# Performance work log

Measured on AMD Instinct MI355X. Metric: run time of the kernel, lower is better.

Reference implementation:

```python
import jax, jax.numpy as jnp
import numpy as np

B, D = 16384, 1024
N_CROSS = 3
EPS = 1e-3  # keras BatchNormalization default epsilon


def _bn(x, gamma, beta, mean, var):
    # inference-mode batch norm over feature axis
    return gamma * (x - mean) * jax.lax.rsqrt(var + EPS) + beta


def setup_inputs() -> dict:
    key = jax.random.key(0)
    ks = jax.random.split(key, 16)
    s = lambda fan_in: 1.0 / np.sqrt(fan_in)
    inp = {
        "x": jax.random.normal(ks[0], (B, D), jnp.float32),
        "cross_w": jax.random.normal(ks[1], (N_CROSS, D), jnp.float32) * s(D),
        "cross_b": jax.random.normal(ks[2], (N_CROSS, D), jnp.float32) * 0.01,
        "w1": jax.random.normal(ks[3], (D, 64), jnp.float32) * s(D),
        "b1": jnp.zeros((64,), jnp.float32),
        "gamma1": jnp.ones((64,), jnp.float32),
        "beta1": jnp.zeros((64,), jnp.float32),
        "mean1": jax.random.normal(ks[4], (64,), jnp.float32) * 0.1,
        "var1": jax.random.uniform(ks[5], (64,), jnp.float32, 0.5, 1.5),
        "w2": jax.random.normal(ks[6], (64, 48), jnp.float32) * s(64),
        "b2": jnp.zeros((48,), jnp.float32),
        "gamma2": jnp.ones((48,), jnp.float32),
        "beta2": jnp.zeros((48,), jnp.float32),
        "mean2": jax.random.normal(ks[7], (48,), jnp.float32) * 0.1,
        "var2": jax.random.uniform(ks[8], (48,), jnp.float32, 0.5, 1.5),
        "w3": jax.random.normal(ks[9], (48, 24), jnp.float32) * s(48),
        "b3": jnp.zeros((24,), jnp.float32),
        "gamma3": jnp.ones((24,), jnp.float32),
        "beta3": jnp.zeros((24,), jnp.float32),
        "mean3": jax.random.normal(ks[10], (24,), jnp.float32) * 0.1,
        "var3": jax.random.uniform(ks[11], (24,), jnp.float32, 0.5, 1.5),
        "w_out": jax.random.normal(ks[12], (D + 24, 1), jnp.float32) * s(D + 24),
        "b_out": jnp.zeros((1,), jnp.float32),
    }
    return inp


def reference(x, cross_w, cross_b, w1, b1, gamma1, beta1, mean1, var1,
              w2, b2, gamma2, beta2, mean2, var2,
              w3, b3, gamma3, beta3, mean3, var3, w_out, b_out):
    # ---- cross network: xl = x0 * (xl . w) + b + xl ----
    # Algebraically identical to matmul(x0[:,:,None], xl[:,None,:]) @ w,
    # computed in O(B*D) instead of materializing [B, D, D].
    x0 = x
    xl = x
    for i in range(N_CROSS):
        scal = jnp.einsum('bd,d->b', xl, cross_w[i])  # [B]
        xl = x0 * scal[:, None] + cross_b[i] + xl
    # ---- deep tower (inference: dropout is identity, BN uses moving stats) ----
    h = _bn(jax.nn.relu(x @ w1 + b1), gamma1, beta1, mean1, var1)
    h = _bn(jnp.tanh(h @ w2 + b2), gamma2, beta2, mean2, var2)
    h = _bn(jnp.tanh(h @ w3 + b3), gamma3, beta3, mean3, var3)
    out = jnp.concatenate([xl, h], axis=1)           # [B, D+24]
    return jax.nn.sigmoid(out @ w_out + b_out)       # [B, 1]
```

## Files before the change

kernel.cpp:

```cpp
#include <hip/hip_runtime.h>
#include <hip/hip_bf16.h>
#include <math.h>

typedef __attribute__((ext_vector_type(8))) short bf16x8;
typedef __attribute__((ext_vector_type(4))) float f32x4;

constexpr int BD = 1024;
constexpr float EPS = 1e-3f;
constexpr int WB_MAIN = 32 * 5 * 64 * 8 * 2;
constexpr int WB2_OFF = WB_MAIN;
constexpr int WB3_OFF = WB2_OFF + 6144;
constexpr int CST_OFF = WB3_OFF + 4096;

__device__ __forceinline__ float wave_allsum(float v) {
#pragma unroll
    for (int m = 1; m < 64; m <<= 1) v += __shfl_xor(v, m, 64);
    return v;
}
__device__ __forceinline__ unsigned short f2bf(float f) {
    __hip_bfloat16 h = __float2bfloat16(f);
    unsigned short u; __builtin_memcpy(&u, &h, 2);
    return u;
}
__device__ __forceinline__ float bf2f(unsigned short u) {
    return __uint_as_float(((unsigned)u) << 16);
}
__device__ __forceinline__ float tanh_fast(float x) {
    const float xc = fminf(fmaxf(x, -15.f), 15.f);
    const float e = __expf(2.f * xc);
    return (e - 1.f) * __builtin_amdgcn_rcpf(e + 1.f);
}
__device__ __forceinline__ float sigmoid_fast(float z) {
    return __builtin_amdgcn_rcpf(1.f + __expf(-z));
}

__global__ void dcn_prep(const float* __restrict__ w1,
                         const float* __restrict__ cross_w,
                         const float* __restrict__ cross_b,
                         const float* __restrict__ w_out,
                         const float* __restrict__ w2,
                         const float* __restrict__ w3,
                         unsigned short* __restrict__ ws) {
    const int bx = blockIdx.x;
    if (bx == 40) {
        if (threadIdx.x < 64) {
            const int l = threadIdx.x;
            float q2 = 0.f, q3 = 0.f, Cc = 0.f;
            for (int j = 0; j < 16; ++j) {
                const int k = l * 16 + j;
                const float c0 = cross_b[k], c1 = cross_b[BD + k], c2 = cross_b[2 * BD + k];
                q2 += c0 * cross_w[BD + k];
                q3 += (c0 + c1) * cross_w[2 * BD + k];
                Cc += (c0 + c1 + c2) * w_out[k];
            }
            q2 = wave_allsum(q2); q3 = wave_allsum(q3); Cc = wave_allsum(Cc);
            float* consts = (float*)((char*)ws + CST_OFF);
            if (l == 0) { consts[0] = q2; consts[1] = q3; consts[2] = Cc; }
        }
        return;
    }
    if (bx < 40) {
        const int idx = bx * 256 + threadIdx.x;
        const int g = idx / 320;
        const int rem = idx - g * 320;
        const int t = rem >> 6;
        const int l = rem & 63;
        const int c = l & 15;
        const int k0 = g * 32 + (l >> 4) * 8;
        unsigned short o[8] __attribute__((aligned(16)));
#pragma unroll
        for (int j = 0; j < 8; ++j) {
            const int k = k0 + j;
            unsigned short r;
            if (t < 4) {
                r = f2bf(w1[k * 64 + t * 16 + c]);
            } else if (c < 8) {
                const int vsel = c & 3;
                const float v = (vsel < 3) ? cross_w[vsel * BD + k] : w_out[k];
                const unsigned short h = f2bf(v);
                r = (c < 4) ? h : f2bf(v - bf2f(h));
            } else {
                r = 0;
            }
            o[j] = r;
        }
        *(uint4*)(ws + (size_t)idx * 8) = *(const uint4*)o;
        return;
    }
    const int slot = (bx - 41) * 256 + threadIdx.x;
    if (slot < 384) {
        const int f = slot >> 6, l = slot & 63;
        const int K = f / 3, T = f % 3;
        const int kb = K * 32 + (l >> 4) * 8;
        const int col = T * 16 + (l & 15);
        unsigned short o[8] __attribute__((aligned(16)));
#pragma unroll
        for (int j = 0; j < 8; ++j) o[j] = f2bf(w2[(kb + j) * 48 + col]);
        unsigned short* wb2 = (unsigned short*)((char*)ws + WB2_OFF);
        *(uint4*)(wb2 + (size_t)slot * 8) = *(const uint4*)o;
    } else if (slot < 640) {
        const int s2 = slot - 384;
        const int f = s2 >> 6, l = s2 & 63;
        const int K = f >> 1, T = f & 1;
        const int kb = K * 32 + (l >> 4) * 8;
        const int col = T * 16 + (l & 15);
        unsigned short o[8] __attribute__((aligned(16)));
#pragma unroll
        for (int j = 0; j < 8; ++j) {
            const int k = kb + j;
            o[j] = (k < 48 && col < 24) ? f2bf(w3[k * 24 + col]) : (unsigned short)0;
        }
        unsigned short* wb3 = (unsigned short*)((char*)ws + WB3_OFF);
        *(uint4*)(wb3 + (size_t)s2 * 8) = *(const uint4*)o;
    }
}

__global__ __launch_bounds__(128, 2) void dcn_main(
    const float* __restrict__ x,
    const unsigned short* __restrict__ wbm,
    const unsigned short* __restrict__ w2f,
    const unsigned short* __restrict__ w3f,
    const float* __restrict__ consts,
    const float* __restrict__ b1, const float* __restrict__ g1,
    const float* __restrict__ be1, const float* __restrict__ m1, const float* __restrict__ v1,
    const float* __restrict__ b2, const float* __restrict__ g2,
    const float* __restrict__ be2, const float* __restrict__ m2, const float* __restrict__ v2,
    const float* __restrict__ b3, const float* __restrict__ g3,
    const float* __restrict__ be3, const float* __restrict__ m3, const float* __restrict__ v3,
    const float* __restrict__ w_out, const float* __restrict__ b_out,
    float* __restrict__ out)
{
    __shared__ char sb[14336] __attribute__((aligned(16)));
    constexpr int RED = 0, H1 = 5120, H2 = 9472, LC = 13824;

    const int tid = threadIdx.x;
    const int l = tid & 63;
    const int w = tid >> 6;
    const int ar = l & 15;
    const int ag = l >> 4;
    const int gr0 = blockIdx.x * 16;

    const float* xbase = x + (size_t)(gr0 + ar) * BD + w * 512 + ag * 8;
    const bf16x8* bb = (const bf16x8*)wbm + (size_t)(w * 16 * 5) * 64 + l;

    float4 A0[8], A1[8];
#pragma unroll
    for (int s = 0; s < 8; ++s) {
        A0[s] = *(const float4*)(xbase + s * 32);
        A1[s] = *(const float4*)(xbase + s * 32 + 4);
    }
    bf16x8 Bf[4][5];
#pragma unroll
    for (int s = 0; s < 4; ++s)
#pragma unroll
        for (int t = 0; t < 5; ++t) Bf[s][t] = bb[(s * 5 + t) * 64];

    f32x4 acc0 = {0.f,0.f,0.f,0.f}, acc1 = acc0, acc2 = acc0, acc3 = acc0, acc4 = acc0;

#pragma unroll
    for (int s = 0; s < 16; ++s) {
        const float4 va0 = A0[s & 7];
        const float4 va1 = A1[s & 7];
        if (s < 8) {
            A0[s & 7] = *(const float4*)(xbase + (s + 8) * 32);
            A1[s & 7] = *(const float4*)(xbase + (s + 8) * 32 + 4);
        }
        const bf16x8 B0 = Bf[s & 3][0], B1 = Bf[s & 3][1], B2 = Bf[s & 3][2],
                     B3 = Bf[s & 3][3], B4 = Bf[s & 3][4];
        if (s + 4 < 16) {
#pragma unroll
            for (int t = 0; t < 5; ++t) Bf[s & 3][t] = bb[((s + 4) * 5 + t) * 64];
        }
        bf16x8 xh, xl;
#define CVT(F, I) { const unsigned short h_ = f2bf(F); xh[I] = (short)h_; \
                    xl[I] = (short)f2bf((F) - bf2f(h_)); }
        CVT(va0.x, 0) CVT(va0.y, 1) CVT(va0.z, 2) CVT(va0.w, 3)
        CVT(va1.x, 4) CVT(va1.y, 5) CVT(va1.z, 6) CVT(va1.w, 7)
#undef CVT
        acc0 = __builtin_amdgcn_mfma_f32_16x16x32_bf16(xh, B0, acc0, 0, 0, 0);
        acc1 = __builtin_amdgcn_mfma_f32_16x16x32_bf16(xh, B1, acc1, 0, 0, 0);
        acc2 = __builtin_amdgcn_mfma_f32_16x16x32_bf16(xh, B2, acc2, 0, 0, 0);
        acc3 = __builtin_amdgcn_mfma_f32_16x16x32_bf16(xh, B3, acc3, 0, 0, 0);
        acc4 = __builtin_amdgcn_mfma_f32_16x16x32_bf16(xh, B4, acc4, 0, 0, 0);
        acc4 = __builtin_amdgcn_mfma_f32_16x16x32_bf16(xl, B4, acc4, 0, 0, 0);
    }

    if (w == 1) {
        *(f32x4*)&sb[RED + 0 * 1024 + l * 16] = acc0;
        *(f32x4*)&sb[RED + 1 * 1024 + l * 16] = acc1;
        *(f32x4*)&sb[RED + 2 * 1024 + l * 16] = acc2;
        *(f32x4*)&sb[RED + 3 * 1024 + l * 16] = acc3;
        *(f32x4*)&sb[RED + 4 * 1024 + l * 16] = acc4;
    }
    __syncthreads();
    if (w == 1) return;

    acc0 += *(const f32x4*)&sb[RED + 0 * 1024 + l * 16];
    acc1 += *(const f32x4*)&sb[RED + 1 * 1024 + l * 16];
    acc2 += *(const f32x4*)&sb[RED + 2 * 1024 + l * 16];
    acc3 += *(const f32x4*)&sb[RED + 3 * 1024 + l * 16];
    acc4 += *(const f32x4*)&sb[RED + 4 * 1024 + l * 16];

    const bf16x8* w2b = (const bf16x8*)w2f + l;
    bf16x8 W2[6];
#pragma unroll
    for (int f = 0; f < 6; ++f) W2[f] = w2b[f * 64];
    const bf16x8* w3b = (const bf16x8*)w3f + l;
    bf16x8 W3[4];
#pragma unroll
    for (int f = 0; f < 4; ++f) W3[f] = w3b[f * 64];

    const float q2c = consts[0], q3c = consts[1], Ccc = consts[2];
    const float bo = b_out[0];
    const float wo0 = w_out[1024 + ar];
    const float wo1 = (ar < 8) ? w_out[1040 + ar] : 0.f;
    float b1p[4], g1p[4], be1p[4], m1p[4], iv1p[4];
#pragma unroll
    for (int t = 0; t < 4; ++t) {
        const int c = t * 16 + ar;
        b1p[t] = b1[c]; g1p[t] = g1[c]; be1p[t] = be1[c]; m1p[t] = m1[c];
        iv1p[t] = rsqrtf(v1[c] + EPS);
    }
    float b2p[3], g2p[3], be2p[3], m2p[3], iv2p[3];
#pragma unroll
    for (int t = 0; t < 3; ++t) {
        const int c = t * 16 + ar;
        b2p[t] = b2[c]; g2p[t] = g2[c]; be2p[t] = be2[c]; m2p[t] = m2[c];
        iv2p[t] = rsqrtf(v2[c] + EPS);
    }
    float b3p[2], g3p[2], be3p[2], m3p[2], iv3p[2];
#pragma unroll
    for (int t = 0; t < 2; ++t) {
        const int c = t == 0 ? ar : (16 + ar < 24 ? 16 + ar : 23);
        b3p[t] = b3[c]; g3p[t] = g3[c]; be3p[t] = be3[c]; m3p[t] = m3[c];
        iv3p[t] = rsqrtf(v3[c] + EPS);
    }

    {
        f32x4 p4 = acc4;
#pragma unroll
        for (int q = 0; q < 4; ++q) p4[q] += __shfl_xor(acc4[q], 4, 64);
        if (ar < 4) {
#pragma unroll
            for (int q = 0; q < 4; ++q)
                *(float*)&sb[LC + ((ag * 4 + q) * 4 + ar) * 4] = p4[q];
        }
    }

    {
        const f32x4 av[4] = {acc0, acc1, acc2, acc3};
#pragma unroll
        for (int t = 0; t < 4; ++t) {
            const int c = t * 16 + ar;
#pragma unroll
            for (int q = 0; q < 4; ++q) {
                const float y = fmaxf(av[t][q] + b1p[t], 0.f);
                const float h = fmaf(g1p[t] * (y - m1p[t]), iv1p[t], be1p[t]);
                *(float*)&sb[H1 + (ag * 4 + q) * 272 + c * 4] = h;
            }
        }
    }
    {
        const f32x4 z4 = {0.f, 0.f, 0.f, 0.f};
        *(f32x4*)&sb[H2 + ar * 272 + 192 + ag * 16] = z4;
    }

    bf16x8 a2[2];
#pragma unroll
    for (int K = 0; K < 2; ++K) {
        const float4 f0 = *(const float4*)&sb[H1 + ar * 272 + (K * 32 + ag * 8) * 4];
        const float4 f1 = *(const float4*)&sb[H1 + ar * 272 + (K * 32 + ag * 8) * 4 + 16];
        const float v[8] = {f0.x, f0.y, f0.z, f0.w, f1.x, f1.y, f1.z, f1.w};
#pragma unroll
        for (int i = 0; i < 8; ++i) a2[K][i] = (short)f2bf(v[i]);
    }
    f32x4 c2t[3] = {{0.f,0.f,0.f,0.f},{0.f,0.f,0.f,0.f},{0.f,0.f,0.f,0.f}};
#pragma unroll
    for (int K = 0; K < 2; ++K) {
        c2t[0] = __builtin_amdgcn_mfma_f32_16x16x32_bf16(a2[K], W2[K * 3 + 0], c2t[0], 0, 0, 0);
        c2t[1] = __builtin_amdgcn_mfma_f32_16x16x32_bf16(a2[K], W2[K * 3 + 1], c2t[1], 0, 0, 0);
        c2t[2] = __builtin_amdgcn_mfma_f32_16x16x32_bf16(a2[K], W2[K * 3 + 2], c2t[2], 0, 0, 0);
    }
#pragma unroll
    for (int t = 0; t < 3; ++t) {
        const int c = t * 16 + ar;
#pragma unroll
        for (int q = 0; q < 4; ++q) {
            const float th = tanh_fast(c2t[t][q] + b2p[t]);
            const float h = fmaf(g2p[t] * (th - m2p[t]), iv2p[t], be2p[t]);
            *(float*)&sb[H2 + (ag * 4 + q) * 272 + c * 4] = h;
        }
    }

    bf16x8 a3[2];
#pragma unroll
    for (int K = 0; K < 2; ++K) {
        const float4 f0 = *(const float4*)&sb[H2 + ar * 272 + (K * 32 + ag * 8) * 4];
        const float4 f1 = *(const float4*)&sb[H2 + ar * 272 + (K * 32 + ag * 8) * 4 + 16];
        const float v[8] = {f0.x, f0.y, f0.z, f0.w, f1.x, f1.y, f1.z, f1.w};
#pragma unroll
        for (int i = 0; i < 8; ++i) a3[K][i] = (short)f2bf(v[i]);
    }
    f32x4 c3t[2] = {{0.f,0.f,0.f,0.f},{0.f,0.f,0.f,0.f}};
#pragma unroll
    for (int K = 0; K < 2; ++K) {
        c3t[0] = __builtin_amdgcn_mfma_f32_16x16x32_bf16(a3[K], W3[K * 2 + 0], c3t[0], 0, 0, 0);
        c3t[1] = __builtin_amdgcn_mfma_f32_16x16x32_bf16(a3[K], W3[K * 2 + 1], c3t[1], 0, 0, 0);
    }
    float contrib[4];
#pragma unroll
    for (int q = 0; q < 4; ++q) {
        const float t0 = tanh_fast(c3t[0][q] + b3p[0]);
        const float h0 = fmaf(g3p[0] * (t0 - m3p[0]), iv3p[0], be3p[0]);
        const float t1 = tanh_fast(c3t[1][q] + b3p[1]);
        const float h1v = fmaf(g3p[1] * (t1 - m3p[1]), iv3p[1], be3p[1]);
        contrib[q] = h0 * wo0 + h1v * wo1;
    }
#pragma unroll
    for (int m = 1; m < 16; m <<= 1) {
#pragma unroll
        for (int q = 0; q < 4; ++q) contrib[q] += __shfl_xor(contrib[q], m, 64);
    }

#pragma unroll
    for (int q = 0; q < 4; ++q) {
        const f32x4 pr = *(const f32x4*)&sb[LC + (ag * 4 + q) * 16];
        const float p1 = pr[0], p2 = pr[1], p3 = pr[2], d0 = pr[3];
        const float s1 = p1;
        const float s2 = fmaf(1.f + s1, p2, q2c);
        const float s3 = fmaf(1.f + s1 + s2, p3, q3c);
        const float alpha = 1.f + s1 + s2 + s3;
        const float z = fmaf(alpha, d0, Ccc) + contrib[q] + bo;
        const float o = sigmoid_fast(z);
        if (ar == q) out[gr0 + ag * 4 + q] = o;
    }
}

extern "C" void kernel_launch(void* const* d_in, const int* in_sizes, int n_in,
                              void* d_out, int out_size, void* d_ws, size_t ws_size,
                              hipStream_t stream) {
    const float* x       = (const float*)d_in[0];
    const float* cross_w = (const float*)d_in[1];
    const float* cross_b = (const float*)d_in[2];
    const float* w1      = (const float*)d_in[3];
    const float* b1      = (const float*)d_in[4];
    const float* g1      = (const float*)d_in[5];
    const float* be1     = (const float*)d_in[6];
    const float* m1      = (const float*)d_in[7];
    const float* v1      = (const float*)d_in[8];
    const float* w2      = (const float*)d_in[9];
    const float* b2      = (const float*)d_in[10];
    const float* g2      = (const float*)d_in[11];
    const float* be2     = (const float*)d_in[12];
    const float* m2      = (const float*)d_in[13];
    const float* v2      = (const float*)d_in[14];
    const float* w3      = (const float*)d_in[15];
    const float* b3      = (const float*)d_in[16];
    const float* g3      = (const float*)d_in[17];
    const float* be3     = (const float*)d_in[18];
    const float* m3      = (const float*)d_in[19];
    const float* v3      = (const float*)d_in[20];
    const float* w_out   = (const float*)d_in[21];
    const float* b_out   = (const float*)d_in[22];
    float* out = (float*)d_out;

    unsigned short* ws = (unsigned short*)d_ws;
    const unsigned short* w2f = (const unsigned short*)((char*)d_ws + WB2_OFF);
    const unsigned short* w3f = (const unsigned short*)((char*)d_ws + WB3_OFF);
    const float* consts = (const float*)((char*)d_ws + CST_OFF);

    dcn_prep<<<44, 256, 0, stream>>>(w1, cross_w, cross_b, w_out, w2, w3, ws);
    dcn_main<<<1024, 128, 0, stream>>>(x, ws, w2f, w3f, consts,
                                       b1, g1, be1, m1, v1,
                                       b2, g2, be2, m2, v2,
                                       b3, g3, be3, m3, v3,
                                       w_out, b_out, out);
}
```

Before: 26.18 us.

## Stage x rows through double-buffered LDS with coalesced row loads

```diff
diff --git a/kernel.cpp b/kernel.cpp
--- a/kernel.cpp
+++ b/kernel.cpp
@@ -11,6 +11,11 @@
 constexpr int WB2_OFF = WB_MAIN;
 constexpr int WB3_OFF = WB2_OFF + 6144;
 constexpr int CST_OFF = WB3_OFF + 4096;
+
+constexpr int ROWB = 528;
+constexpr int BUFB = 16 * ROWB;
+constexpr int WAVEB = 2 * BUFB;
+constexpr int H1 = 0, H2 = 4352, LC = 8704, RED = WAVEB;
 
 __device__ __forceinline__ float wave_allsum(float v) {
 #pragma unroll
@@ -130,8 +135,7 @@
     const float* __restrict__ w_out, const float* __restrict__ b_out,
     float* __restrict__ out)
 {
-    __shared__ char sb[14336] __attribute__((aligned(16)));
-    constexpr int RED = 0, H1 = 5120, H2 = 9472, LC = 13824;
+    __shared__ char sb[2 * WAVEB] __attribute__((aligned(16)));
 
     const int tid = threadIdx.x;
     const int l = tid & 63;
@@ -139,43 +143,47 @@
     const int ar = l & 15;
     const int ag = l >> 4;
     const int gr0 = blockIdx.x * 16;
-
-    const float* xbase = x + (size_t)(gr0 + ar) * BD + w * 512 + ag * 8;
+    const int woff = w * WAVEB;
+
+    const int srow = l >> 5;
+    const int scol = (l & 31) * 4;
+    const float* xw = x + (size_t)(gr0 + srow) * BD + w * 512 + scol;
+    char* cdst = &sb[woff + srow * ROWB + scol * 4];
+
+    float4 S[8];
+    auto stage = [&](int c) {
+#pragma unroll
+        for (int i = 0; i < 8; ++i)
+            S[i] = *(const float4*)(xw + (size_t)(i * 2) * BD + c * 128);
+    };
+    auto commit = [&](int c) {
+        char* d = cdst + (c & 1) * BUFB;
+#pragma unroll
+        for (int i = 0; i < 8; ++i)
+            *(float4*)(d + i * 2 * ROWB) = S[i];
+    };
+
     const bf16x8* bb = (const bf16x8*)wbm + (size_t)(w * 16 * 5) * 64 + l;
-
-    float4 A0[8], A1[8];
-#pragma unroll
-    for (int s = 0; s < 8; ++s) {
-        A0[s] = *(const float4*)(xbase + s * 32);
-        A1[s] = *(const float4*)(xbase + s * 32 + 4);
-    }
     bf16x8 Bf[4][5];
-#pragma unroll
-    for (int s = 0; s < 4; ++s)
-#pragma unroll
-        for (int t = 0; t < 5; ++t) Bf[s][t] = bb[(s * 5 + t) * 64];
 
     f32x4 acc0 = {0.f,0.f,0.f,0.f}, acc1 = acc0, acc2 = acc0, acc3 = acc0, acc4 = acc0;
 
-#pragma unroll
-    for (int s = 0; s < 16; ++s) {
-        const float4 va0 = A0[s & 7];
-        const float4 va1 = A1[s & 7];
-        if (s < 8) {
-            A0[s & 7] = *(const float4*)(xbase + (s + 8) * 32);
-            A1[s & 7] = *(const float4*)(xbase + (s + 8) * 32 + 4);
-        }
-        const bf16x8 B0 = Bf[s & 3][0], B1 = Bf[s & 3][1], B2 = Bf[s & 3][2],
-                     B3 = Bf[s & 3][3], B4 = Bf[s & 3][4];
-        if (s + 4 < 16) {
-#pragma unroll
-            for (int t = 0; t < 5; ++t) Bf[s & 3][t] = bb[((s + 4) * 5 + t) * 64];
+    const int abase = woff + ar * ROWB + ag * 32;
+    auto kstep = [&](int g_lin, int cbuf) {
+        const int s = g_lin & 3;
+        const float4 a0 = *(const float4*)&sb[abase + cbuf + s * 128];
+        const float4 a1 = *(const float4*)&sb[abase + cbuf + s * 128 + 16];
+        const bf16x8 B0 = Bf[g_lin & 3][0], B1 = Bf[g_lin & 3][1], B2 = Bf[g_lin & 3][2],
+                     B3 = Bf[g_lin & 3][3], B4 = Bf[g_lin & 3][4];
+        if (g_lin + 4 < 16) {
+#pragma unroll
+            for (int t = 0; t < 5; ++t) Bf[g_lin & 3][t] = bb[((g_lin + 4) * 5 + t) * 64];
         }
         bf16x8 xh, xl;
 #define CVT(F, I) { const unsigned short h_ = f2bf(F); xh[I] = (short)h_; \
                     xl[I] = (short)f2bf((F) - bf2f(h_)); }
-        CVT(va0.x, 0) CVT(va0.y, 1) CVT(va0.z, 2) CVT(va0.w, 3)
-        CVT(va1.x, 4) CVT(va1.y, 5) CVT(va1.z, 6) CVT(va1.w, 7)
+        CVT(a0.x, 0) CVT(a0.y, 1) CVT(a0.z, 2) CVT(a0.w, 3)
+        CVT(a1.x, 4) CVT(a1.y, 5) CVT(a1.z, 6) CVT(a1.w, 7)
 #undef CVT
         acc0 = __builtin_amdgcn_mfma_f32_16x16x32_bf16(xh, B0, acc0, 0, 0, 0);
         acc1 = __builtin_amdgcn_mfma_f32_16x16x32_bf16(xh, B1, acc1, 0, 0, 0);
@@ -183,7 +191,28 @@
         acc3 = __builtin_amdgcn_mfma_f32_16x16x32_bf16(xh, B3, acc3, 0, 0, 0);
         acc4 = __builtin_amdgcn_mfma_f32_16x16x32_bf16(xh, B4, acc4, 0, 0, 0);
         acc4 = __builtin_amdgcn_mfma_f32_16x16x32_bf16(xl, B4, acc4, 0, 0, 0);
-    }
+    };
+
+    stage(0);
+#pragma unroll
+    for (int i = 0; i < 4; ++i)
+#pragma unroll
+        for (int t = 0; t < 5; ++t) Bf[i][t] = bb[(i * 5 + t) * 64];
+    commit(0);
+    stage(1);
+#pragma unroll
+    for (int s = 0; s < 4; ++s) kstep(s, 0);
+    commit(1);
+    stage(2);
+#pragma unroll
+    for (int s = 0; s < 4; ++s) kstep(4 + s, BUFB);
+    commit(2);
+    stage(3);
+#pragma unroll
+    for (int s = 0; s < 4; ++s) kstep(8 + s, 0);
+    commit(3);
+#pragma unroll
+    for (int s = 0; s < 4; ++s) kstep(12 + s, BUFB);
 
     if (w == 1) {
         *(f32x4*)&sb[RED + 0 * 1024 + l * 16] = acc0;
```

Result: slower. 36.79 us (+40.6%).
